# Optimization experiments

Hardware: AMD Instinct MI355X
Metric: run time of the kernel (lower is better)

Reference implementation:

```python
import jax, jax.numpy as jnp
import numpy as np

B, N, D = 2, 2048, 1024
RANK, HEADS = 256, 16
HS = RANK // HEADS          # 16, low-rank head size for QK
DH = D // HEADS             # 64, value head size
SCALE = 1.0 / np.sqrt(HS)


def setup_inputs() -> dict:
    key = jax.random.key(0)
    k1, k2, k3 = jax.random.split(key, 3)
    x = jax.random.normal(k1, (B, N, D), dtype=jnp.float32)
    # causal additive mask, 0 on/below diag, -1e9 above
    mask = jnp.where(jnp.tril(jnp.ones((N, N), dtype=bool)), 0.0, -1e9).astype(jnp.float32)
    Wqk = jax.random.normal(k2, (2 * RANK, D), dtype=jnp.float32) * (1.0 / np.sqrt(D))
    Wv = jax.random.normal(k3, (D, D), dtype=jnp.float32) * (1.0 / np.sqrt(D))
    return {"x": x, "mask": mask, "Wqk": Wqk, "Wv": Wv}


def reference(x, mask, Wqk, Wv):
    b, n, d = x.shape
    qk = jnp.einsum('bnd,rd->bnr', x, Wqk)            # [b,n,2*rank]
    q, k = jnp.split(qk, 2, axis=-1)                  # [b,n,rank] each
    # L2 normalize over FULL rank dim (before head split), clamp norm >= 1e-6
    q = q / jnp.maximum(jnp.linalg.norm(q, axis=-1, keepdims=True), 1e-6)
    k = k / jnp.maximum(jnp.linalg.norm(k, axis=-1, keepdims=True), 1e-6)
    q = q.reshape(b, n, HEADS, HS).transpose(0, 2, 1, 3)   # [b,h,n,hs]
    k = k.reshape(b, n, HEADS, HS).transpose(0, 2, 1, 3)
    v = jnp.einsum('bnd,ed->bne', x, Wv).reshape(b, n, HEADS, DH).transpose(0, 2, 1, 3)  # [b,h,n,dh]
    att = jnp.einsum('bhqe,bhke->bhqk', q, k) * SCALE
    att = jnp.clip(att, -10000.0, 10000.0)
    att = att + mask[None, None, :, :]
    att = jax.nn.softmax(att, axis=-1)
    # NaN guard: zero NaNs then renormalize (no-op when no NaNs)
    att = jnp.where(jnp.isnan(att), 0.0, att)
    att = att / jnp.maximum(att.sum(axis=-1, keepdims=True), 1e-6)
    y = jnp.einsum('bhqk,bhkd->bhqd', att, v)              # [b,h,n,dh]
    return y.transpose(0, 2, 1, 3).reshape(b, n, d)
```

## Files before the change

kernel.cpp:

```cpp
#include <hip/hip_runtime.h>
#include <math.h>

#define BATCH 2
#define SEQ   2048
#define DIM   1024
#define RANK  256
#define HEADS 16
#define HS    16
#define DH    64
#define MROWS 4096

#define QSCALE 0.36067376f

typedef __attribute__((ext_vector_type(8)))  short    short8;
typedef __attribute__((ext_vector_type(4)))  float    f32x4;
typedef __attribute__((ext_vector_type(16))) float    f32x16;
typedef __attribute__((ext_vector_type(2)))  unsigned uint2v;

#define GPTR const __attribute__((address_space(1))) unsigned int*
#define LPTR __attribute__((address_space(3))) unsigned int*

__device__ __forceinline__ unsigned short f2bf(float f) {
    union { float f; unsigned u; } v; v.f = f;
    return (unsigned short)((v.u + 0x7FFFu + ((v.u >> 16) & 1u)) >> 16);
}
__device__ __forceinline__ float bf2f(unsigned short h) {
    union { unsigned u; float f; } v; v.u = ((unsigned)h) << 16;
    return v.f;
}

__device__ __forceinline__ float exp2_poly(float x) {
    return fmaf(x, fmaf(x, fmaf(x, 0.05550411f, 0.24022651f), 0.69314718f), 1.0f);
}

#define XQ   1048576
#define WQKQ 131072
#define WVQ  262144
__global__ __launch_bounds__(256) void conv3(const float* __restrict__ x,
                                             const float* __restrict__ wqk,
                                             const float* __restrict__ wv,
                                             unsigned short* __restrict__ xb,
                                             unsigned short* __restrict__ wcat)
{
    const int i = blockIdx.x * 256 + threadIdx.x;
    const float* src; unsigned short* dst; int j;
    if (i < XQ)              { src = x;   dst = xb;   j = i; }
    else if (i < XQ + WQKQ)  { src = wqk; dst = wcat; j = i - XQ; }
    else                     { src = wv;  dst = wcat + (size_t)4 * WQKQ; j = i - XQ - WQKQ; }
    float4 v = ((const float4*)src)[j];
    ushort4 o; o.x = f2bf(v.x); o.y = f2bf(v.y); o.z = f2bf(v.z); o.w = f2bf(v.w);
    ((ushort4*)dst)[j] = o;
}

__global__ __launch_bounds__(256, 3) void gemm_mfma(const unsigned short* __restrict__ A,
                                                    const unsigned short* __restrict__ W,
                                                    unsigned short* __restrict__ qkb,
                                                    unsigned short* __restrict__ vt)
{
    __shared__ __align__(16) unsigned short Alds[2][128 * 64];
    __shared__ __align__(16) unsigned short Blds[2][64 * 64];

    const int tid = threadIdx.x;
    const int w = tid >> 6, lane = tid & 63;
    const int lr = lane & 15, lg = lane >> 4;
    const int wm = w >> 1, wn = w & 1;

    const int Lf = blockIdx.x;
    const int xcd = Lf & 7;
    const int i5 = Lf >> 3;
    const int bm = (4 * xcd + (i5 & 3)) * 128;
    const int bn = (i5 >> 2) * 64;

    const int rs = lane >> 3, cs = lane & 7;

    f32x4 acc[4][2] = {};

#define STAGEG(kt_, buf_) do {                                                        \
        const int k0_ = (kt_) * 64;                                                   \
        _Pragma("unroll")                                                             \
        for (int i = 0; i < 4; ++i) {                                                 \
            const int r = w * 32 + i * 8 + rs;                                        \
            __builtin_amdgcn_global_load_lds(                                         \
                (GPTR)&A[(size_t)(bm + r) * 1024 + k0_ + 8 * (cs ^ (r & 7))],         \
                (LPTR)&Alds[buf_][(w * 32 + i * 8) * 64], 16, 0, 0);                  \
        }                                                                             \
        _Pragma("unroll")                                                             \
        for (int i = 0; i < 2; ++i) {                                                 \
            const int r = w * 16 + i * 8 + rs;                                        \
            __builtin_amdgcn_global_load_lds(                                         \
                (GPTR)&W[(size_t)(bn + r) * 1024 + k0_ + 8 * (cs ^ (r & 7))],         \
                (LPTR)&Blds[buf_][(w * 16 + i * 8) * 64], 16, 0, 0);                  \
        }                                                                             \
    } while (0)

    STAGEG(0, 0);

    #pragma unroll 1
    for (int kt = 0; kt < 16; ++kt) {
        if (kt + 1 < 16) {
            STAGEG(kt + 1, (kt + 1) & 1);
            asm volatile("s_waitcnt vmcnt(6)" ::: "memory");
        } else {
            asm volatile("s_waitcnt vmcnt(0)" ::: "memory");
        }
        __builtin_amdgcn_sched_barrier(0);
        __builtin_amdgcn_s_barrier();

        const int buf = kt & 1;
        #pragma unroll
        for (int kk = 0; kk < 2; ++kk) {
            short8 af[4], bfr[2];
            #pragma unroll
            for (int mi = 0; mi < 4; ++mi) {
                const int row = wm * 64 + mi * 16 + lr;
                af[mi] = *(const short8*)&Alds[buf][row * 64 + 8 * ((kk * 4 + lg) ^ (row & 7))];
            }
            #pragma unroll
            for (int ni = 0; ni < 2; ++ni) {
                const int row = wn * 32 + ni * 16 + lr;
                bfr[ni] = *(const short8*)&Blds[buf][row * 64 + 8 * ((kk * 4 + lg) ^ (row & 7))];
            }
            #pragma unroll
            for (int mi = 0; mi < 4; ++mi)
                #pragma unroll
                for (int ni = 0; ni < 2; ++ni)
                    acc[mi][ni] = __builtin_amdgcn_mfma_f32_16x16x32_bf16(af[mi], bfr[ni], acc[mi][ni], 0, 0, 0);
        }
        __builtin_amdgcn_s_barrier();
    }
#undef STAGEG

    if (bn < 512) {
        #pragma unroll
        for (int mi = 0; mi < 4; ++mi) {
            const int rbase = bm + wm * 64 + mi * 16 + lg * 4;
            #pragma unroll
            for (int ni = 0; ni < 2; ++ni) {
                const int col = bn + wn * 32 + ni * 16 + lr;
                #pragma unroll
                for (int r = 0; r < 4; ++r)
                    qkb[(size_t)(rbase + r) * 512 + col] = f2bf(acc[mi][ni][r]);
            }
        }
    } else {
        const int nb = bn - 512;
        #pragma unroll
        for (int mi = 0; mi < 4; ++mi) {
            const int m = bm + wm * 64 + mi * 16 + lg * 4;
            const int bb = m >> 11, ms = m & 2047;
            #pragma unroll
            for (int ni = 0; ni < 2; ++ni) {
                const int d = nb + wn * 32 + ni * 16 + lr;
                ushort4 pk;
                pk.x = f2bf(acc[mi][ni][0]); pk.y = f2bf(acc[mi][ni][1]);
                pk.z = f2bf(acc[mi][ni][2]); pk.w = f2bf(acc[mi][ni][3]);
                *(ushort4*)&vt[((size_t)bb * DIM + d) * SEQ + ms] = pk;
            }
        }
    }
}

__global__ __launch_bounds__(256) void l2norm_split(const unsigned short* __restrict__ qkb,
                                                    unsigned short* __restrict__ qn,
                                                    unsigned short* __restrict__ kn)
{
    const int row = blockIdx.x;
    const int t = threadIdx.x;
    const unsigned short* p = qkb + (size_t)row * 512;
    float q = bf2f(p[t]);
    float k = bf2f(p[t + 256]);
    float sq = q * q, sk = k * k;
    #pragma unroll
    for (int off = 32; off > 0; off >>= 1) {
        sq += __shfl_down(sq, off);
        sk += __shfl_down(sk, off);
    }
    __shared__ float sh[8];
    const int wid = t >> 6;
    if ((t & 63) == 0) { sh[wid * 2] = sq; sh[wid * 2 + 1] = sk; }
    __syncthreads();
    sq = sh[0] + sh[2] + sh[4] + sh[6];
    sk = sh[1] + sh[3] + sh[5] + sh[7];
    const float rq = QSCALE / fmaxf(sqrtf(sq), 1e-6f);
    const float rk = 1.0f   / fmaxf(sqrtf(sk), 1e-6f);

    const int b = row >> 11, n = row & 2047;
    const int head = t >> 4, hs = t & 15;
    const size_t o = (((size_t)b * HEADS + head) * SEQ + n) * 16 + hs;
    qn[o] = f2bf(q * rq);
    kn[o] = f2bf(k * rk);
}


template<bool MASK>
__device__ __forceinline__ void qpv(const short8 ak0, const short8 ak1, const short8 bq,
                                    const short8 vb[4][2], int kb, int hi, int qg,
                                    f32x16 o[2], float& lp)
{
    const f32x16 z = {};
    short8 pa[4];

    const f32x16 s0 = __builtin_amdgcn_mfma_f32_32x32x16_bf16(ak0, bq, z, 0, 0, 0);
    const f32x16 s1 = __builtin_amdgcn_mfma_f32_32x32x16_bf16(ak1, bq, z, 0, 0, 0);

    float p0[16], p1[16];
    #pragma unroll
    for (int r = 0; r < 16; ++r) {
        float e0 = exp2_poly(s0[r]);
        float e1 = exp2_poly(s1[r]);
        if (MASK) {
            const int kl = kb + (r & 3) + 8 * (r >> 2) + 4 * hi;
            e0 = (kl > qg) ? 0.0f : e0;
            e1 = (kl + 32 > qg) ? 0.0f : e1;
        }
        p0[r] = e0; p1[r] = e1;
        lp += e0 + e1;
    }

    #pragma unroll
    for (int g = 0; g < 4; ++g) {
        const float* pc = (g < 2) ? p0 : p1;
        const int jj = 2 * (g & 1);
        unsigned a0, a1, b0, b1;
        asm("v_cvt_pk_bf16_f32 %0, %1, %2" : "=v"(a0) : "v"(pc[4*jj]),     "v"(pc[4*jj + 1]));
        asm("v_cvt_pk_bf16_f32 %0, %1, %2" : "=v"(b0) : "v"(pc[4*jj + 2]), "v"(pc[4*jj + 3]));
        asm("v_cvt_pk_bf16_f32 %0, %1, %2" : "=v"(a1) : "v"(pc[4*jj + 4]), "v"(pc[4*jj + 5]));
        asm("v_cvt_pk_bf16_f32 %0, %1, %2" : "=v"(b1) : "v"(pc[4*jj + 6]), "v"(pc[4*jj + 7]));
        const uint2v r0 = __builtin_amdgcn_permlane32_swap(a0, a1, false, false);
        const uint2v r1 = __builtin_amdgcn_permlane32_swap(b0, b1, false, false);
        union { short8 s; unsigned u[4]; } pu;
        pu.u[0] = r0[0]; pu.u[1] = r1[0]; pu.u[2] = r0[1]; pu.u[3] = r1[1];
        pa[g] = pu.s;
    }

    #pragma unroll
    for (int g = 0; g < 4; ++g)
        #pragma unroll
        for (int half = 0; half < 2; ++half)
            o[half] = __builtin_amdgcn_mfma_f32_32x32x16_bf16(pa[g], vb[g][half], o[half], 0, 0, 0);
}

__device__ __forceinline__ void qdisp(bool last, const short8 ak0, const short8 ak1,
                                      const short8 bq, const short8 vb[4][2], int kb,
                                      int hi, int qmin, int qg,
                                      f32x16 o[2], float& lp)
{
    if (!last) {
        qpv<false>(ak0, ak1, bq, vb, kb, hi, qg, o, lp);
    } else if (kb <= qmin + 31) {
        if (kb + 63 <= qmin) qpv<false>(ak0, ak1, bq, vb, kb, hi, qg, o, lp);
        else                 qpv<true >(ak0, ak1, bq, vb, kb, hi, qg, o, lp);
    }
}

__global__ __launch_bounds__(256, 2) void attn_q64(const unsigned short* __restrict__ qn,
                                                   const unsigned short* __restrict__ kn,
                                                   const unsigned short* __restrict__ vt,
                                                   float* __restrict__ out)
{
    const int L = blockIdx.x;
    const int bh = L & 31;
    const int p  = L >> 5;
    const int h = bh & 15, b = bh >> 4;

    const int tid = threadIdx.x, w = tid >> 6, lane = tid & 63;
    const int seg = w >> 1, kh = w & 1;
    const int l31 = lane & 31, hi = lane >> 5;

    const int qt  = seg ? p : 31 - p;
    const int nts = (qt >> 1) + 1;
    const int nt0 = ((31 - p) >> 1) + 1;
    const int qmin0 = qt * 64, qmin1 = qt * 64 + 32;
    const int qg0 = qmin0 + l31, qg1 = qmin1 + l31;

    __shared__ __align__(16) unsigned char smem[33792];

    const unsigned short* qbh = qn + (size_t)bh * SEQ * 16;
    const unsigned short* kbh = kn + (size_t)bh * SEQ * 16;

    const short8 bq0 = *(const short8*)&qbh[qg0 * 16 + 8 * hi];
    const short8 bq1 = *(const short8*)&qbh[qg1 * 16 + 8 * hi];

    f32x16 o0[2] = {}, o1[2] = {};
    float lp0 = 0.0f, lp1 = 0.0f;

    const unsigned short* kwin = kbh + (64 * kh + l31) * 16 + 8 * hi;
    short8 ak0 = *(const short8*)(kwin);
    short8 ak1 = *(const short8*)(kwin + 32 * 16);

    const int vsub = lane >> 4, vslot = lane & 15;

#define STAGEV(kt_, buf_) do {                                                                    \
        const int k0_ = (kt_) * 128;                                                              \
        _Pragma("unroll")                                                                         \
        for (int i = 0; i < 4; ++i) {                                                             \
            const int c = 4 * w + i;                                                              \
            const int dh = 4 * c + vsub;                                                          \
            const int so = 8 * (vslot ^ (dh & 15));                                               \
            __builtin_amdgcn_global_load_lds(                                                     \
                (GPTR)&vt[((size_t)b * DIM + h * DH + dh) * SEQ + k0_ + so],                      \
                (LPTR)(smem + (buf_) * 16384 + c * 1024), 16, 0, 0);                              \
        }                                                                                         \
    } while (0)

    STAGEV(0, 0);

    #pragma unroll 1
    for (int kt = 0; kt < nt0; ++kt) {
        short8 an0 = ak0, an1 = ak1;
        if (kt + 1 < nt0) {
            STAGEV(kt + 1, (kt + 1) & 1);
            an0 = *(const short8*)(kwin + (size_t)(kt + 1) * 128 * 16);
            an1 = *(const short8*)(kwin + (size_t)(kt + 1) * 128 * 16 + 32 * 16);
            asm volatile("s_waitcnt vmcnt(6)" ::: "memory");
        } else {
            asm volatile("s_waitcnt vmcnt(0)" ::: "memory");
        }
        __builtin_amdgcn_sched_barrier(0);
        __builtin_amdgcn_s_barrier();

        if (kt < nts) {
            const unsigned short* Vs = (const unsigned short*)(smem + (kt & 1) * 16384);
            const int kb = kt * 128 + 64 * kh;

            short8 vb[4][2];
            #pragma unroll
            for (int g = 0; g < 4; ++g)
                #pragma unroll
                for (int half = 0; half < 2; ++half) {
                    const int row = half * 32 + l31;
                    const int slot = (8 * kh + 2 * g + hi) ^ (row & 15);
                    vb[g][half] = *(const short8*)&Vs[row * 128 + 8 * slot];
                }

            const bool last = (kt == nts - 1);
            __builtin_amdgcn_s_setprio(1);
            qdisp(last, ak0, ak1, bq0, vb, kb, hi, qmin0, qg0, o0, lp0);
            qdisp(last, ak0, ak1, bq1, vb, kb, hi, qmin1, qg1, o1, lp1);
            __builtin_amdgcn_s_setprio(0);
        }

        ak0 = an0; ak1 = an1;
        __builtin_amdgcn_s_barrier();
    }
#undef STAGEV

    lp0 += __shfl_xor(lp0, 32);
    lp1 += __shfl_xor(lp1, 32);

    __syncthreads();
    float* Os = (float*)smem;
    float* Ls = (float*)(smem + 32768);

    if (kh == 1) {
        #pragma unroll
        for (int half = 0; half < 2; ++half)
            #pragma unroll
            for (int r = 0; r < 16; ++r) {
                const int q = (r & 3) + 8 * (r >> 2) + 4 * hi;
                Os[(seg * 64 + q) * 64 + half * 32 + l31]      = o0[half][r];
                Os[(seg * 64 + 32 + q) * 64 + half * 32 + l31] = o1[half][r];
            }
        Ls[seg * 128 + lane]      = lp0;
        Ls[seg * 128 + 64 + lane] = lp1;
    }
    __syncthreads();
    if (kh == 0) {
        float lt0 = lp0 + Ls[seg * 128 + lane];
        float lt1 = lp1 + Ls[seg * 128 + 64 + lane];
        const float inv0 = 1.0f / fmaxf(lt0, 1e-6f);
        const float inv1 = 1.0f / fmaxf(lt1, 1e-6f);
        #pragma unroll
        for (int r = 0; r < 16; ++r) {
            const int q = (r & 3) + 8 * (r >> 2) + 4 * hi;
            const float iv0 = __shfl(inv0, q);
            const float iv1 = __shfl(inv1, q);
            #pragma unroll
            for (int half = 0; half < 2; ++half) {
                const float v0 = (o0[half][r] + Os[(seg * 64 + q) * 64 + half * 32 + l31]) * iv0;
                const float v1 = (o1[half][r] + Os[(seg * 64 + 32 + q) * 64 + half * 32 + l31]) * iv1;
                __builtin_nontemporal_store(v0,
                    &out[((size_t)b * SEQ + qmin0 + q) * DIM + h * DH + half * 32 + l31]);
                __builtin_nontemporal_store(v1,
                    &out[((size_t)b * SEQ + qmin1 + q) * DIM + h * DH + half * 32 + l31]);
            }
        }
    }
}

extern "C" void kernel_launch(void* const* d_in, const int* in_sizes, int n_in,
                              void* d_out, int out_size, void* d_ws, size_t ws_size,
                              hipStream_t stream)
{
    const float* x   = (const float*)d_in[0];
    const float* Wqk = (const float*)d_in[2];
    const float* Wv  = (const float*)d_in[3];
    float* out = (float*)d_out;

    unsigned short* xb   = (unsigned short*)d_ws;
    unsigned short* qkb  = xb  + (size_t)MROWS * DIM;
    unsigned short* vt   = qkb + (size_t)MROWS * 512;
    unsigned short* wcat = vt  + (size_t)BATCH * DIM * SEQ;
    unsigned short* qn = xb;
    unsigned short* kn = xb + (size_t)32 * SEQ * 16;

    conv3<<<5632, 256, 0, stream>>>(x, Wqk, Wv, xb, wcat);
    gemm_mfma<<<768, 256, 0, stream>>>(xb, wcat, qkb, vt);
    l2norm_split<<<MROWS, 256, 0, stream>>>(qkb, qn, kn);
    attn_q64<<<512, 256, 0, stream>>>(qn, kn, vt, out);
}
```

Before: 65.86 us.

## Fuse L2-norm into GEMM epilogue via atomic row norms, apply scaling in attention

Removes the separate l2norm_split kernel. The GEMM epilogue now writes unnormalized Q/K straight into the head-major layout and accumulates squared row norms with atomicAdd into a buffer that conv3 zeroes. The attention kernel reads these norms and rescales the Q and K fragments in registers before the MFMA. This saves one launch and one read-write pass over the QK buffer. In exchange it adds atomics, scattered 2-byte stores in the GEMM, per-tile rescaling ALU work and extra loads in the attention loop, and a second bf16 rounding step.

```diff
diff --git a/kernel.cpp b/kernel.cpp
--- a/kernel.cpp
+++ b/kernel.cpp
@@ -33,16 +33,38 @@
     return fmaf(x, fmaf(x, fmaf(x, 0.05550411f, 0.24022651f), 0.69314718f), 1.0f);
 }
 
+__device__ __forceinline__ short8 fold8(short8 v, float s) {
+    union { short8 v8; unsigned short us[8]; } u; u.v8 = v;
+    float f[8];
+    #pragma unroll
+    for (int j = 0; j < 8; ++j) f[j] = bf2f(u.us[j]) * s;
+    unsigned w0, w1, w2, w3;
+    asm("v_cvt_pk_bf16_f32 %0, %1, %2" : "=v"(w0) : "v"(f[0]), "v"(f[1]));
+    asm("v_cvt_pk_bf16_f32 %0, %1, %2" : "=v"(w1) : "v"(f[2]), "v"(f[3]));
+    asm("v_cvt_pk_bf16_f32 %0, %1, %2" : "=v"(w2) : "v"(f[4]), "v"(f[5]));
+    asm("v_cvt_pk_bf16_f32 %0, %1, %2" : "=v"(w3) : "v"(f[6]), "v"(f[7]));
+    union { short8 v8; unsigned uu[4]; } o;
+    o.uu[0] = w0; o.uu[1] = w1; o.uu[2] = w2; o.uu[3] = w3;
+    return o.v8;
+}
+
 #define XQ   1048576
 #define WQKQ 131072
 #define WVQ  262144
+#define NTOT (XQ + WQKQ + WVQ)
 __global__ __launch_bounds__(256) void conv3(const float* __restrict__ x,
                                              const float* __restrict__ wqk,
                                              const float* __restrict__ wv,
                                              unsigned short* __restrict__ xb,
-                                             unsigned short* __restrict__ wcat)
+                                             unsigned short* __restrict__ wcat,
+                                             float* __restrict__ norms)
 {
     const int i = blockIdx.x * 256 + threadIdx.x;
+    if (i >= NTOT) {
+        const int j = i - NTOT;
+        ((float4*)norms)[j] = make_float4(0.f, 0.f, 0.f, 0.f);
+        return;
+    }
     const float* src; unsigned short* dst; int j;
     if (i < XQ)              { src = x;   dst = xb;   j = i; }
     else if (i < XQ + WQKQ)  { src = wqk; dst = wcat; j = i - XQ; }
@@ -54,8 +76,11 @@
 
 __global__ __launch_bounds__(256, 3) void gemm_mfma(const unsigned short* __restrict__ A,
                                                     const unsigned short* __restrict__ W,
-                                                    unsigned short* __restrict__ qkb,
-                                                    unsigned short* __restrict__ vt)
+                                                    unsigned short* __restrict__ qh,
+                                                    unsigned short* __restrict__ khm,
+                                                    unsigned short* __restrict__ vt,
+                                                    float* __restrict__ nq,
+                                                    float* __restrict__ nk)
 {
     __shared__ __align__(16) unsigned short Alds[2][128 * 64];
     __shared__ __align__(16) unsigned short Blds[2][64 * 64];
@@ -131,15 +156,31 @@
 #undef STAGEG
 
     if (bn < 512) {
+        const bool isq = (bn < 256);
+        float* nbuf = isq ? nq : nk;
+        unsigned short* dst = isq ? qh : khm;
         #pragma unroll
         for (int mi = 0; mi < 4; ++mi) {
             const int rbase = bm + wm * 64 + mi * 16 + lg * 4;
             #pragma unroll
+            for (int r = 0; r < 4; ++r) {
+                float t = acc[mi][0][r] * acc[mi][0][r] + acc[mi][1][r] * acc[mi][1][r];
+                t += __shfl_xor(t, 1);
+                t += __shfl_xor(t, 2);
+                t += __shfl_xor(t, 4);
+                t += __shfl_xor(t, 8);
+                if (lr == 0) atomicAdd(&nbuf[rbase + r], t);
+            }
+            #pragma unroll
             for (int ni = 0; ni < 2; ++ni) {
                 const int col = bn + wn * 32 + ni * 16 + lr;
+                const int h = (col & 255) >> 4;
                 #pragma unroll
-                for (int r = 0; r < 4; ++r)
-                    qkb[(size_t)(rbase + r) * 512 + col] = f2bf(acc[mi][ni][r]);
+                for (int r = 0; r < 4; ++r) {
+                    const int row = rbase + r;
+                    const int bb = row >> 11, ns = row & 2047;
+                    dst[(((size_t)bb * HEADS + h) * SEQ + ns) * 16 + lr] = f2bf(acc[mi][ni][r]);
+                }
             }
         }
     } else {
@@ -158,37 +199,6 @@
             }
         }
     }
-}
-
-__global__ __launch_bounds__(256) void l2norm_split(const unsigned short* __restrict__ qkb,
-                                                    unsigned short* __restrict__ qn,
-                                                    unsigned short* __restrict__ kn)
-{
-    const int row = blockIdx.x;
-    const int t = threadIdx.x;
-    const unsigned short* p = qkb + (size_t)row * 512;
-    float q = bf2f(p[t]);
-    float k = bf2f(p[t + 256]);
-    float sq = q * q, sk = k * k;
-    #pragma unroll
-    for (int off = 32; off > 0; off >>= 1) {
-        sq += __shfl_down(sq, off);
-        sk += __shfl_down(sk, off);
-    }
-    __shared__ float sh[8];
-    const int wid = t >> 6;
-    if ((t & 63) == 0) { sh[wid * 2] = sq; sh[wid * 2 + 1] = sk; }
-    __syncthreads();
-    sq = sh[0] + sh[2] + sh[4] + sh[6];
-    sk = sh[1] + sh[3] + sh[5] + sh[7];
-    const float rq = QSCALE / fmaxf(sqrtf(sq), 1e-6f);
-    const float rk = 1.0f   / fmaxf(sqrtf(sk), 1e-6f);
-
-    const int b = row >> 11, n = row & 2047;
-    const int head = t >> 4, hs = t & 15;
-    const size_t o = (((size_t)b * HEADS + head) * SEQ + n) * 16 + hs;
-    qn[o] = f2bf(q * rq);
-    kn[o] = f2bf(k * rk);
 }
 
 
@@ -253,9 +263,11 @@
     }
 }
 
-__global__ __launch_bounds__(256, 2) void attn_q64(const unsigned short* __restrict__ qn,
-                                                   const unsigned short* __restrict__ kn,
+__global__ __launch_bounds__(256, 2) void attn_q64(const unsigned short* __restrict__ qh,
+                                                   const unsigned short* __restrict__ khm,
                                                    const unsigned short* __restrict__ vt,
+                                                   const float* __restrict__ nq,
+                                                   const float* __restrict__ nk,
                                                    float* __restrict__ out)
 {
     const int L = blockIdx.x;
@@ -275,18 +287,23 @@
 
     __shared__ __align__(16) unsigned char smem[33792];
 
-    const unsigned short* qbh = qn + (size_t)bh * SEQ * 16;
-    const unsigned short* kbh = kn + (size_t)bh * SEQ * 16;
-
-    const short8 bq0 = *(const short8*)&qbh[qg0 * 16 + 8 * hi];
-    const short8 bq1 = *(const short8*)&qbh[qg1 * 16 + 8 * hi];
+    const unsigned short* qbh = qh  + (size_t)bh * SEQ * 16;
+    const unsigned short* kbh = khm + (size_t)bh * SEQ * 16;
+
+    const float rq0 = QSCALE / fmaxf(sqrtf(nq[b * SEQ + qg0]), 1e-6f);
+    const float rq1 = QSCALE / fmaxf(sqrtf(nq[b * SEQ + qg1]), 1e-6f);
+    const short8 bq0 = fold8(*(const short8*)&qbh[qg0 * 16 + 8 * hi], rq0);
+    const short8 bq1 = fold8(*(const short8*)&qbh[qg1 * 16 + 8 * hi], rq1);
 
     f32x16 o0[2] = {}, o1[2] = {};
     float lp0 = 0.0f, lp1 = 0.0f;
 
     const unsigned short* kwin = kbh + (64 * kh + l31) * 16 + 8 * hi;
+    const float* nkb = nk + b * SEQ + 64 * kh + l31;
     short8 ak0 = *(const short8*)(kwin);
     short8 ak1 = *(const short8*)(kwin + 32 * 16);
+    float nk0c = nkb[0];
+    float nk1c = nkb[32];
 
     const int vsub = lane >> 4, vslot = lane & 15;
 
@@ -308,11 +325,14 @@
     #pragma unroll 1
     for (int kt = 0; kt < nt0; ++kt) {
         short8 an0 = ak0, an1 = ak1;
+        float nk0n = nk0c, nk1n = nk1c;
         if (kt + 1 < nt0) {
             STAGEV(kt + 1, (kt + 1) & 1);
             an0 = *(const short8*)(kwin + (size_t)(kt + 1) * 128 * 16);
             an1 = *(const short8*)(kwin + (size_t)(kt + 1) * 128 * 16 + 32 * 16);
-            asm volatile("s_waitcnt vmcnt(6)" ::: "memory");
+            nk0n = nkb[(kt + 1) * 128];
+            nk1n = nkb[(kt + 1) * 128 + 32];
+            asm volatile("s_waitcnt vmcnt(8)" ::: "memory");
         } else {
             asm volatile("s_waitcnt vmcnt(0)" ::: "memory");
         }
@@ -322,6 +342,11 @@
         if (kt < nts) {
             const unsigned short* Vs = (const unsigned short*)(smem + (kt & 1) * 16384);
             const int kb = kt * 128 + 64 * kh;
+
+            const float rk0 = 1.0f / fmaxf(sqrtf(nk0c), 1e-6f);
+            const float rk1 = 1.0f / fmaxf(sqrtf(nk1c), 1e-6f);
+            const short8 af0 = fold8(ak0, rk0);
+            const short8 af1 = fold8(ak1, rk1);
 
             short8 vb[4][2];
             #pragma unroll
@@ -335,12 +360,13 @@
 
             const bool last = (kt == nts - 1);
             __builtin_amdgcn_s_setprio(1);
-            qdisp(last, ak0, ak1, bq0, vb, kb, hi, qmin0, qg0, o0, lp0);
-            qdisp(last, ak0, ak1, bq1, vb, kb, hi, qmin1, qg1, o1, lp1);
+            qdisp(last, af0, af1, bq0, vb, kb, hi, qmin0, qg0, o0, lp0);
+            qdisp(last, af0, af1, bq1, vb, kb, hi, qmin1, qg1, o1, lp1);
             __builtin_amdgcn_s_setprio(0);
         }
 
         ak0 = an0; ak1 = an1;
+        nk0c = nk0n; nk1c = nk1n;
         __builtin_amdgcn_s_barrier();
     }
 #undef STAGEV
@@ -398,14 +424,15 @@
     float* out = (float*)d_out;
 
     unsigned short* xb   = (unsigned short*)d_ws;
-    unsigned short* qkb  = xb  + (size_t)MROWS * DIM;
-    unsigned short* vt   = qkb + (size_t)MROWS * 512;
-    unsigned short* wcat = vt  + (size_t)BATCH * DIM * SEQ;
-    unsigned short* qn = xb;
-    unsigned short* kn = xb + (size_t)32 * SEQ * 16;
-
-    conv3<<<5632, 256, 0, stream>>>(x, Wqk, Wv, xb, wcat);
-    gemm_mfma<<<768, 256, 0, stream>>>(xb, wcat, qkb, vt);
-    l2norm_split<<<MROWS, 256, 0, stream>>>(qkb, qn, kn);
-    attn_q64<<<512, 256, 0, stream>>>(qn, kn, vt, out);
-}
+    unsigned short* vt   = xb   + (size_t)MROWS * DIM;
+    unsigned short* wcat = vt   + (size_t)BATCH * DIM * SEQ;
+    unsigned short* qh   = wcat + (size_t)1536 * DIM;
+    unsigned short* khm  = qh   + (size_t)32 * SEQ * 16;
+    float* norms = (float*)(khm + (size_t)32 * SEQ * 16);
+    float* nq = norms;
+    float* nk = norms + MROWS;
+
+    conv3<<<5640, 256, 0, stream>>>(x, Wqk, Wv, xb, wcat, norms);
+    gemm_mfma<<<768, 256, 0, stream>>>(xb, wcat, qh, khm, vt, nq, nk);
+    attn_q64<<<512, 256, 0, stream>>>(qh, khm, vt, nq, nk, out);
+}
```

Measured after the change: 62.94 us. 4.4% less time.
